# Performance work log

Hardware: AMD Instinct MI355X
Metric: run time of the kernel (lower is better)

Reference implementation:

```python
import jax, jax.numpy as jnp
import numpy as np

EPS = 1e-06
H = 25  # num heads


def _rmsnorm(x, w, eps=EPS):
    # normalize over last dim in float32, as in the torch module
    xf = x.astype(jnp.float32)
    var = jnp.mean(xf * xf, axis=-1, keepdims=True)
    return (w * (xf * jax.lax.rsqrt(var + eps))).astype(x.dtype)


def setup_inputs() -> dict:
    key = jax.random.key(0)
    ks = jax.random.split(key, 4)
    B, N, C = 8, 1025, 3200
    x = jax.random.normal(ks[0], (B, N, C), dtype=jnp.float32)
    qkv_w = jax.random.normal(ks[1], (C, 3 * C), dtype=jnp.float32) * (C ** -0.5)
    qkv_b = jnp.zeros((3 * C,), dtype=jnp.float32)
    q_norm_w = jnp.ones((C,), dtype=jnp.float32)
    k_norm_w = jnp.ones((C,), dtype=jnp.float32)
    proj_w = jax.random.normal(ks[2], (C, C), dtype=jnp.float32) * (C ** -0.5)
    proj_b = jnp.zeros((C,), dtype=jnp.float32)
    return {"x": x, "qkv_w": qkv_w, "qkv_b": qkv_b, "q_norm_w": q_norm_w,
            "k_norm_w": k_norm_w, "proj_w": proj_w, "proj_b": proj_b}


def reference(x, qkv_w, qkv_b, q_norm_w, k_norm_w, proj_w, proj_b):
    B, N, C = x.shape
    D = C // H
    scale = D ** -0.5
    qkv = x @ qkv_w + qkv_b                      # [B, N, 3C]
    q, k, v = jnp.split(qkv, 3, axis=-1)         # each [B, N, C]
    # QK RMSNorm is over the FULL embed_dim (heads flattened), per source.
    q = _rmsnorm(q, q_norm_w)
    k = _rmsnorm(k, k_norm_w)
    q = q.reshape(B, N, H, D)
    k = k.reshape(B, N, H, D)
    v = v.reshape(B, N, H, D)
    attn = jnp.einsum('bqhd,bkhd->bhqk', q * scale, k)   # [B, H, N, N]
    attn = jax.nn.softmax(attn, axis=-1)
    out = jnp.einsum('bhqk,bkhd->bqhd', attn, v).reshape(B, N, C)
    return out @ proj_w + proj_b
```

## Files before the change

### kernel.cpp

```cpp
#include <hip/hip_runtime.h>
#include <hip/hip_bf16.h>
#include <math.h>

#define B_ 8
#define N_ 1025
#define C_ 3200
#define H_ 25
#define D_ 128
#define M_ (B_ * N_)
#define C3_ (3 * C_)

typedef unsigned short u16;
typedef unsigned int u32;
typedef short bf16x8 __attribute__((ext_vector_type(8)));
typedef float f32x4 __attribute__((ext_vector_type(4)));

__device__ inline void load_lds16(const void* g, void* s) {
    __builtin_amdgcn_global_load_lds(
        (const __attribute__((address_space(1))) void*)g,
        (__attribute__((address_space(3))) void*)s, 16, 0, 0);
}

__device__ inline void split_pair(float x0, float x1, u32& hpk, u32& lpk) {
    __hip_bfloat162 h2 = __float22bfloat162_rn(float2{x0, x1});
    union { __hip_bfloat162 b; u32 u; } cv; cv.b = h2;
    u32 h = cv.u;
    float hf0 = __uint_as_float(h << 16);
    float hf1 = __uint_as_float(h & 0xFFFF0000u);
    __hip_bfloat162 l2 = __float22bfloat162_rn(float2{x0 - hf0, x1 - hf1});
    union { __hip_bfloat162 b; u32 u; } cl; cl.b = l2;
    hpk = h; lpk = cl.u;
}

__device__ inline void split1(float x, u16& h, u16& l) {
    union { __hip_bfloat16 b; u16 u; } ch, cl;
    ch.b = __float2bfloat16(x);
    float hf = __uint_as_float(((u32)ch.u) << 16);
    cl.b = __float2bfloat16(x - hf);
    h = ch.u; l = cl.u;
}

__global__ __launch_bounds__(256) void gemm_split(
    const float* __restrict__ A, const float* __restrict__ Bm,
    const float* __restrict__ bias, float* __restrict__ Cc,
    int M, int N)
{
    __shared__ u16  As_hi[128 * 32];
    __shared__ u16  As_lo[128 * 32];
    __shared__ float Bf[32 * 128];

    const int tid  = threadIdx.x;
    const int lane = tid & 63;
    const int w    = tid >> 6;
    const int wm   = w & 1, wn = w >> 1;
    const int rowBase = blockIdx.y * 128;
    const int colBase = blockIdx.x * 128;
    const int lr = lane & 15, lg = lane >> 4;

    const int ar = tid >> 3;
    const int ak = (tid & 7) * 4;

    f32x4 acc[4][4] = {};

    for (int k0 = 0; k0 < C_; k0 += 32) {
        #pragma unroll
        for (int p = 0; p < 4; ++p) {
            int c = p * 256 + tid;
            const float* g = Bm + (size_t)(k0 + (c >> 5)) * N
                                + colBase + (c & 31) * 4;
            load_lds16(g, &Bf[(p * 256 + w * 64) * 4]);
        }
        #pragma unroll
        for (int p = 0; p < 4; ++p) {
            int r  = p * 32 + ar;
            int gr = rowBase + r; if (gr >= M) gr = M - 1;
            float4 a4 = *(const float4*)(A + (size_t)gr * C_ + k0 + ak);
            u32 h0, h1, l0, l1;
            split_pair(a4.x, a4.y, h0, l0);
            split_pair(a4.z, a4.w, h1, l1);
            *(uint2*)&As_hi[r * 32 + ak] = make_uint2(h0, h1);
            *(uint2*)&As_lo[r * 32 + ak] = make_uint2(l0, l1);
        }
        __syncthreads();

        bf16x8 ah[4], al[4];
        #pragma unroll
        for (int i = 0; i < 4; ++i) {
            ah[i] = *(const bf16x8*)&As_hi[(wm * 64 + i * 16 + lr) * 32 + lg * 8];
            al[i] = *(const bf16x8*)&As_lo[(wm * 64 + i * 16 + lr) * 32 + lg * 8];
        }
        #pragma unroll
        for (int j = 0; j < 4; ++j) {
            const float* bp = &Bf[(lg * 8) * 128 + wn * 64 + j * 16 + lr];
            union { u32 u[4]; bf16x8 v; } BH, BL;
            split_pair(bp[0 * 128], bp[1 * 128], BH.u[0], BL.u[0]);
            split_pair(bp[2 * 128], bp[3 * 128], BH.u[1], BL.u[1]);
            split_pair(bp[4 * 128], bp[5 * 128], BH.u[2], BL.u[2]);
            split_pair(bp[6 * 128], bp[7 * 128], BH.u[3], BL.u[3]);
            #pragma unroll
            for (int i = 0; i < 4; ++i)
                acc[i][j] = __builtin_amdgcn_mfma_f32_16x16x32_bf16(
                    ah[i], BH.v, acc[i][j], 0, 0, 0);
            #pragma unroll
            for (int i = 0; i < 4; ++i)
                acc[i][j] = __builtin_amdgcn_mfma_f32_16x16x32_bf16(
                    al[i], BH.v, acc[i][j], 0, 0, 0);
            #pragma unroll
            for (int i = 0; i < 4; ++i)
                acc[i][j] = __builtin_amdgcn_mfma_f32_16x16x32_bf16(
                    ah[i], BL.v, acc[i][j], 0, 0, 0);
        }
        __syncthreads();
    }

    #pragma unroll
    for (int i = 0; i < 4; ++i) {
        #pragma unroll
        for (int j = 0; j < 4; ++j) {
            int gc = colBase + wn * 64 + j * 16 + lr;
            float bv = bias[gc];
            #pragma unroll
            for (int r = 0; r < 4; ++r) {
                int gr = rowBase + wm * 64 + i * 16 + lg * 4 + r;
                if (gr < M) Cc[(size_t)gr * N + gc] = acc[i][j][r] + bv;
            }
        }
    }
}

__global__ __launch_bounds__(256) void rmsnorm_kernel(
    float* __restrict__ qkv, const float* __restrict__ qw,
    const float* __restrict__ kw)
{
    const int row   = blockIdx.x >> 1;
    const int which = blockIdx.x & 1;
    float* p = qkv + (size_t)row * C3_ + which * C_;
    const float* w = which ? kw : qw;
    const int tid = threadIdx.x;

    float ss = 0.f;
    for (int i = tid; i < C_; i += 256) {
        float v = p[i];
        ss += v * v;
    }
    #pragma unroll
    for (int off = 32; off; off >>= 1) ss += __shfl_down(ss, off);

    __shared__ float wsum[4];
    __shared__ float stot;
    if ((tid & 63) == 0) wsum[tid >> 6] = ss;
    __syncthreads();
    if (tid == 0) stot = wsum[0] + wsum[1] + wsum[2] + wsum[3];
    __syncthreads();

    const float scale = rsqrtf(stot / (float)C_ + 1e-6f);
    for (int i = tid; i < C_; i += 256) p[i] = p[i] * scale * w[i];
}

__global__ __launch_bounds__(256, 2) void flash_mfma(
    const float* __restrict__ qkv, float* __restrict__ attn_out)
{
    __shared__ u16 Kh[4][32][32];
    __shared__ u16 Kl[4][32][32];
    __shared__ u16 Vth[128][40];
    __shared__ u16 Vtl[128][40];
    __shared__ u16 Ph[4][16][40];
    __shared__ u16 Pl[4][16][40];

    const int b   = blockIdx.z;
    const int h   = blockIdx.y;
    const int q0  = blockIdx.x * 64;
    const int tid = threadIdx.x;
    const int lane = tid & 63;
    const int w    = tid >> 6;
    const int lr = lane & 15, lg = lane >> 4;
    const float scale = 0.088388347648318447f;

    bf16x8 qh[4], ql[4];
    {
        int qr = q0 + w * 16 + lr;
        if (qr >= N_) qr = N_ - 1;
        const float* qp = qkv + (size_t)(b * N_ + qr) * C3_ + h * D_;
        #pragma unroll
        for (int c = 0; c < 4; ++c) {
            float4 x0 = *(const float4*)(qp + c * 32 + lg * 8);
            float4 x1 = *(const float4*)(qp + c * 32 + lg * 8 + 4);
            union { u32 u[4]; bf16x8 v; } Hq, Lq;
            split_pair(x0.x * scale, x0.y * scale, Hq.u[0], Lq.u[0]);
            split_pair(x0.z * scale, x0.w * scale, Hq.u[1], Lq.u[1]);
            split_pair(x1.x * scale, x1.y * scale, Hq.u[2], Lq.u[2]);
            split_pair(x1.z * scale, x1.w * scale, Hq.u[3], Lq.u[3]);
            qh[c] = Hq.v; ql[c] = Lq.v;
        }
    }

    const float* Kbase = qkv + (size_t)b * N_ * C3_ + C_ + h * D_;
    const float* Vbase = qkv + (size_t)b * N_ * C3_ + 2 * C_ + h * D_;

    const int skr = tid >> 3;
    const int skd = (tid & 7) * 16;
    const int svk = (tid & 15) * 2;
    const int svd = (tid >> 4) * 4;

    float4 kg[4], vg[2][2];

    auto stage_load = [&](int kt) {
        int kk = kt * 32 + skr;
        if (kk < N_) {
            const float* p = Kbase + (size_t)kk * C3_ + skd;
            kg[0] = *(const float4*)(p + 0);
            kg[1] = *(const float4*)(p + 4);
            kg[2] = *(const float4*)(p + 8);
            kg[3] = *(const float4*)(p + 12);
        } else {
            kg[0] = kg[1] = kg[2] = kg[3] = make_float4(0.f, 0.f, 0.f, 0.f);
        }
        #pragma unroll
        for (int r = 0; r < 2; ++r) {
            int vk = kt * 32 + svk + r;
            if (vk < N_) {
                const float* p = Vbase + (size_t)vk * C3_ + svd;
                vg[0][r] = *(const float4*)(p);
                vg[1][r] = *(const float4*)(p + 64);
            } else {
                vg[0][r] = make_float4(0.f, 0.f, 0.f, 0.f);
                vg[1][r] = make_float4(0.f, 0.f, 0.f, 0.f);
            }
        }
    };

    auto stage_store = [&]() {
        #pragma unroll
        for (int i = 0; i < 4; ++i) {
            int d = skd + i * 4;
            int c = d >> 5, dd = d & 31;
            u32 h0, l0, h1, l1;
            split_pair(kg[i].x, kg[i].y, h0, l0);
            split_pair(kg[i].z, kg[i].w, h1, l1);
            *(uint2*)&Kh[c][skr][dd] = make_uint2(h0, h1);
            *(uint2*)&Kl[c][skr][dd] = make_uint2(l0, l1);
        }
        #pragma unroll
        for (int half = 0; half < 2; ++half) {
            float a0[4] = { vg[half][0].x, vg[half][0].y, vg[half][0].z, vg[half][0].w };
            float a1[4] = { vg[half][1].x, vg[half][1].y, vg[half][1].z, vg[half][1].w };
            #pragma unroll
            for (int i = 0; i < 4; ++i) {
                int d = svd + half * 64 + i;
                u32 hp, lp;
                split_pair(a0[i], a1[i], hp, lp);
                *(u32*)&Vth[d][svk] = hp;
                *(u32*)&Vtl[d][svk] = lp;
            }
        }
    };

    f32x4 oacc[8] = {};
    float m[4]    = { -INFINITY, -INFINITY, -INFINITY, -INFINITY };
    float lsum[4] = { 0.f, 0.f, 0.f, 0.f };

    const int nkt = (N_ + 31) / 32;
    stage_load(0);
    for (int kt = 0; kt < nkt; ++kt) {
        __syncthreads();
        stage_store();
        __syncthreads();
        if (kt + 1 < nkt) stage_load(kt + 1);

        f32x4 s0 = {}, s1 = {};
        #pragma unroll
        for (int c = 0; c < 4; ++c) {
            bf16x8 kh0 = *(const bf16x8*)&Kh[c][lr][lg * 8];
            bf16x8 kl0 = *(const bf16x8*)&Kl[c][lr][lg * 8];
            bf16x8 kh1 = *(const bf16x8*)&Kh[c][16 + lr][lg * 8];
            bf16x8 kl1 = *(const bf16x8*)&Kl[c][16 + lr][lg * 8];
            s0 = __builtin_amdgcn_mfma_f32_16x16x32_bf16(qh[c], kh0, s0, 0, 0, 0);
            s0 = __builtin_amdgcn_mfma_f32_16x16x32_bf16(ql[c], kh0, s0, 0, 0, 0);
            s0 = __builtin_amdgcn_mfma_f32_16x16x32_bf16(qh[c], kl0, s0, 0, 0, 0);
            s1 = __builtin_amdgcn_mfma_f32_16x16x32_bf16(qh[c], kh1, s1, 0, 0, 0);
            s1 = __builtin_amdgcn_mfma_f32_16x16x32_bf16(ql[c], kh1, s1, 0, 0, 0);
            s1 = __builtin_amdgcn_mfma_f32_16x16x32_bf16(qh[c], kl1, s1, 0, 0, 0);
        }

        const int kb = kt * 32;
        const bool v0 = (kb + lr) < N_;
        const bool v1 = (kb + 16 + lr) < N_;
        #pragma unroll
        for (int r = 0; r < 4; ++r) {
            if (!v0) s0[r] = -INFINITY;
            if (!v1) s1[r] = -INFINITY;
        }

        #pragma unroll
        for (int r = 0; r < 4; ++r) {
            float mt = fmaxf(s0[r], s1[r]);
            mt = fmaxf(mt, __shfl_xor(mt, 1));
            mt = fmaxf(mt, __shfl_xor(mt, 2));
            mt = fmaxf(mt, __shfl_xor(mt, 4));
            mt = fmaxf(mt, __shfl_xor(mt, 8));
            float mn = fmaxf(m[r], mt);
            float al = __expf(m[r] - mn);
            m[r] = mn;
            float p0 = __expf(s0[r] - mn);
            float p1 = __expf(s1[r] - mn);
            float ls = p0 + p1;
            ls += __shfl_xor(ls, 1);
            ls += __shfl_xor(ls, 2);
            ls += __shfl_xor(ls, 4);
            ls += __shfl_xor(ls, 8);
            lsum[r] = lsum[r] * al + ls;
            #pragma unroll
            for (int dt = 0; dt < 8; ++dt) oacc[dt][r] *= al;

            u16 hh, ll;
            split1(p0, hh, ll);
            Ph[w][lg * 4 + r][lr] = hh;
            Pl[w][lg * 4 + r][lr] = ll;
            split1(p1, hh, ll);
            Ph[w][lg * 4 + r][16 + lr] = hh;
            Pl[w][lg * 4 + r][16 + lr] = ll;
        }

        bf16x8 pah = *(const bf16x8*)&Ph[w][lr][lg * 8];
        bf16x8 pal = *(const bf16x8*)&Pl[w][lr][lg * 8];
        #pragma unroll
        for (int dt = 0; dt < 8; ++dt) {
            bf16x8 vh = *(const bf16x8*)&Vth[dt * 16 + lr][lg * 8];
            bf16x8 vl = *(const bf16x8*)&Vtl[dt * 16 + lr][lg * 8];
            oacc[dt] = __builtin_amdgcn_mfma_f32_16x16x32_bf16(pah, vh, oacc[dt], 0, 0, 0);
            oacc[dt] = __builtin_amdgcn_mfma_f32_16x16x32_bf16(pal, vh, oacc[dt], 0, 0, 0);
            oacc[dt] = __builtin_amdgcn_mfma_f32_16x16x32_bf16(pah, vl, oacc[dt], 0, 0, 0);
        }
    }

    #pragma unroll
    for (int r = 0; r < 4; ++r) {
        int q = q0 + w * 16 + lg * 4 + r;
        if (q < N_) {
            float inv = 1.f / lsum[r];
            float* op = attn_out + (size_t)(b * N_ + q) * C_ + h * D_ + lr;
            #pragma unroll
            for (int dt = 0; dt < 8; ++dt) op[dt * 16] = oacc[dt][r] * inv;
        }
    }
}

extern "C" void kernel_launch(void* const* d_in, const int* in_sizes, int n_in,
                              void* d_out, int out_size, void* d_ws, size_t ws_size,
                              hipStream_t stream)
{
    const float* x        = (const float*)d_in[0];
    const float* qkv_w    = (const float*)d_in[1];
    const float* qkv_b    = (const float*)d_in[2];
    const float* q_norm_w = (const float*)d_in[3];
    const float* k_norm_w = (const float*)d_in[4];
    const float* proj_w   = (const float*)d_in[5];
    const float* proj_b   = (const float*)d_in[6];
    float* out = (float*)d_out;

    float* qkv      = (float*)d_ws;
    float* attn_out = qkv + (size_t)M_ * C3_;

    dim3 blk(256);

    gemm_split<<<dim3(C3_ / 128, (M_ + 127) / 128), blk, 0, stream>>>(
        x, qkv_w, qkv_b, qkv, M_, C3_);

    rmsnorm_kernel<<<dim3(M_ * 2), blk, 0, stream>>>(qkv, q_norm_w, k_norm_w);

    flash_mfma<<<dim3((N_ + 63) / 64, H_, B_), blk, 0, stream>>>(qkv, attn_out);

    gemm_split<<<dim3(C_ / 128, (M_ + 127) / 128), blk, 0, stream>>>(
        attn_out, proj_w, proj_b, out, M_, C_);
}
```

Measured before the change: 4.000 ms.

## Pre-split GEMM operands to bf16 hi/lo in workspace and use direct-to-LDS MFMA GEMM

New measurement: 3.999 ms. Within noise of the previous version (-0.0%).

```diff
diff --git a/kernel.cpp b/kernel.cpp
--- a/kernel.cpp
+++ b/kernel.cpp
@@ -40,6 +40,133 @@
     h = ch.u; l = cl.u;
 }
 
+__global__ __launch_bounds__(256) void convert_split(
+    const float4* __restrict__ in, uint2* __restrict__ hi,
+    uint2* __restrict__ lo, int n4)
+{
+    int i = blockIdx.x * 256 + threadIdx.x;
+    if (i < n4) {
+        float4 v = in[i];
+        u32 h0, l0, h1, l1;
+        split_pair(v.x, v.y, h0, l0);
+        split_pair(v.z, v.w, h1, l1);
+        hi[i] = make_uint2(h0, h1);
+        lo[i] = make_uint2(l0, l1);
+    }
+}
+
+__global__ __launch_bounds__(256) void convert_tsplit(
+    const float* __restrict__ in, u16* __restrict__ hi, u16* __restrict__ lo,
+    int K, int Nn)
+{
+    __shared__ float T[32][33];
+    const int tid = threadIdx.x;
+    const int nb = blockIdx.x * 32, kb = blockIdx.y * 32;
+    #pragma unroll
+    for (int p = 0; p < 4; ++p) {
+        int k = p * 8 + (tid >> 5), n = tid & 31;
+        T[k][n] = in[(size_t)(kb + k) * Nn + nb + n];
+    }
+    __syncthreads();
+    const int nn = tid >> 3, k0 = (tid & 7) * 4;
+    u32 h0, l0, h1, l1;
+    split_pair(T[k0][nn], T[k0 + 1][nn], h0, l0);
+    split_pair(T[k0 + 2][nn], T[k0 + 3][nn], h1, l1);
+    size_t o = (size_t)(nb + nn) * K + kb + k0;
+    *(uint2*)&hi[o] = make_uint2(h0, h1);
+    *(uint2*)&lo[o] = make_uint2(l0, l1);
+}
+
+__global__ __launch_bounds__(256) void gemm_bf16split(
+    const u16* __restrict__ Ah, const u16* __restrict__ Al,
+    const u16* __restrict__ Bh, const u16* __restrict__ Bl,
+    const float* __restrict__ bias, float* __restrict__ Cc,
+    int M, int N)
+{
+    __shared__ u16 As_h[4][128][8];
+    __shared__ u16 As_l[4][128][8];
+    __shared__ u16 Bs_h[4][128][8];
+    __shared__ u16 Bs_l[4][128][8];
+
+    const int tid  = threadIdx.x;
+    const int lane = tid & 63;
+    const int w    = tid >> 6;
+    const int wm   = w & 1, wn = w >> 1;
+    const int lr = lane & 15, lg = lane >> 4;
+
+    const int gX   = gridDim.x;
+    const int nwg  = gX * gridDim.y;
+    const int orig = blockIdx.y * gX + blockIdx.x;
+    const int q8 = nwg >> 3, r8 = nwg & 7;
+    const int xcd = orig & 7, oi = orig >> 3;
+    const int wg = (xcd < r8 ? xcd * (q8 + 1)
+                             : r8 * (q8 + 1) + (xcd - r8) * q8) + oi;
+    const int rowBase = (wg / gX) * 128;
+    const int colBase = (wg % gX) * 128;
+
+    f32x4 acc[4][4] = {};
+
+    for (int k0 = 0; k0 < C_; k0 += 32) {
+        #pragma unroll
+        for (int p = 0; p < 2; ++p) {
+            int c   = p * 256 + tid;
+            int row = c & 127, kc = c >> 7;
+            int ldsOff = (p * 256 + w * 64) * 8;
+            int ar = rowBase + row; if (ar >= M) ar = M - 1;
+            size_t aoff = (size_t)ar * C_ + k0 + kc * 8;
+            size_t boff = (size_t)(colBase + row) * C_ + k0 + kc * 8;
+            load_lds16(Ah + aoff, (u16*)As_h + ldsOff);
+            load_lds16(Al + aoff, (u16*)As_l + ldsOff);
+            load_lds16(Bh + boff, (u16*)Bs_h + ldsOff);
+            load_lds16(Bl + boff, (u16*)Bs_l + ldsOff);
+        }
+        __syncthreads();
+
+        bf16x8 ah[4], al[4], bh[4], bl[4];
+        #pragma unroll
+        for (int i = 0; i < 4; ++i) {
+            ah[i] = *(const bf16x8*)&As_h[lg][wm * 64 + i * 16 + lr][0];
+            al[i] = *(const bf16x8*)&As_l[lg][wm * 64 + i * 16 + lr][0];
+            bh[i] = *(const bf16x8*)&Bs_h[lg][wn * 64 + i * 16 + lr][0];
+            bl[i] = *(const bf16x8*)&Bs_l[lg][wn * 64 + i * 16 + lr][0];
+        }
+
+        #pragma unroll
+        for (int j = 0; j < 4; ++j)
+            #pragma unroll
+            for (int i = 0; i < 4; ++i)
+                acc[i][j] = __builtin_amdgcn_mfma_f32_16x16x32_bf16(
+                    ah[i], bh[j], acc[i][j], 0, 0, 0);
+        #pragma unroll
+        for (int j = 0; j < 4; ++j)
+            #pragma unroll
+            for (int i = 0; i < 4; ++i)
+                acc[i][j] = __builtin_amdgcn_mfma_f32_16x16x32_bf16(
+                    al[i], bh[j], acc[i][j], 0, 0, 0);
+        #pragma unroll
+        for (int j = 0; j < 4; ++j)
+            #pragma unroll
+            for (int i = 0; i < 4; ++i)
+                acc[i][j] = __builtin_amdgcn_mfma_f32_16x16x32_bf16(
+                    ah[i], bl[j], acc[i][j], 0, 0, 0);
+        __syncthreads();
+    }
+
+    #pragma unroll
+    for (int i = 0; i < 4; ++i) {
+        #pragma unroll
+        for (int j = 0; j < 4; ++j) {
+            int gc = colBase + wn * 64 + j * 16 + lr;
+            float bv = bias[gc];
+            #pragma unroll
+            for (int r = 0; r < 4; ++r) {
+                int gr = rowBase + wm * 64 + i * 16 + lg * 4 + r;
+                if (gr < M) Cc[(size_t)gr * N + gc] = acc[i][j][r] + bv;
+            }
+        }
+    }
+}
+
 __global__ __launch_bounds__(256) void gemm_split(
     const float* __restrict__ A, const float* __restrict__ Bm,
     const float* __restrict__ bias, float* __restrict__ Cc,
@@ -139,9 +266,9 @@
     const int tid = threadIdx.x;
 
     float ss = 0.f;
-    for (int i = tid; i < C_; i += 256) {
-        float v = p[i];
-        ss += v * v;
+    for (int i = tid; i < C_ / 4; i += 256) {
+        float4 v = ((const float4*)p)[i];
+        ss += v.x * v.x + v.y * v.y + v.z * v.z + v.w * v.w;
     }
     #pragma unroll
     for (int off = 32; off; off >>= 1) ss += __shfl_down(ss, off);
@@ -154,7 +281,13 @@
     __syncthreads();
 
     const float scale = rsqrtf(stot / (float)C_ + 1e-6f);
-    for (int i = tid; i < C_; i += 256) p[i] = p[i] * scale * w[i];
+    for (int i = tid; i < C_ / 4; i += 256) {
+        float4 v  = ((const float4*)p)[i];
+        float4 wv = ((const float4*)w)[i];
+        v.x *= scale * wv.x; v.y *= scale * wv.y;
+        v.z *= scale * wv.z; v.w *= scale * wv.w;
+        ((float4*)p)[i] = v;
+    }
 }
 
 __global__ __launch_bounds__(256, 2) void flash_mfma(
@@ -358,18 +491,50 @@
     const float* proj_b   = (const float*)d_in[6];
     float* out = (float*)d_out;
 
+    const size_t fQ = (size_t)M_ * C3_;
+    const size_t fA = (size_t)M_ * C_;
+    const size_t uW = (size_t)C3_ * C_;
+
     float* qkv      = (float*)d_ws;
-    float* attn_out = qkv + (size_t)M_ * C3_;
+    float* attn_out = qkv + fQ;
+
+    const size_t need = (fQ + fA) * 4 + fA * 2 * 2 + uW * 2 * 2;
 
     dim3 blk(256);
 
-    gemm_split<<<dim3(C3_ / 128, (M_ + 127) / 128), blk, 0, stream>>>(
-        x, qkv_w, qkv_b, qkv, M_, C3_);
-
-    rmsnorm_kernel<<<dim3(M_ * 2), blk, 0, stream>>>(qkv, q_norm_w, k_norm_w);
-
-    flash_mfma<<<dim3((N_ + 63) / 64, H_, B_), blk, 0, stream>>>(qkv, attn_out);
-
-    gemm_split<<<dim3(C_ / 128, (M_ + 127) / 128), blk, 0, stream>>>(
-        attn_out, proj_w, proj_b, out, M_, C_);
-}
+    if (ws_size >= need) {
+        u16* xh = (u16*)(attn_out + fA);
+        u16* xl = xh + fA;
+        u16* wh = xl + fA;
+        u16* wl = wh + uW;
+
+        const int n4 = (int)(fA / 4);
+
+        convert_split<<<dim3((n4 + 255) / 256), blk, 0, stream>>>(
+            (const float4*)x, (uint2*)xh, (uint2*)xl, n4);
+        convert_tsplit<<<dim3(C3_ / 32, C_ / 32), blk, 0, stream>>>(
+            qkv_w, wh, wl, C_, C3_);
+
+        gemm_bf16split<<<dim3(C3_ / 128, (M_ + 127) / 128), blk, 0, stream>>>(
+            xh, xl, wh, wl, qkv_b, qkv, M_, C3_);
+
+        rmsnorm_kernel<<<dim3(M_ * 2), blk, 0, stream>>>(qkv, q_norm_w, k_norm_w);
+
+        flash_mfma<<<dim3((N_ + 63) / 64, H_, B_), blk, 0, stream>>>(qkv, attn_out);
+
+        convert_split<<<dim3((n4 + 255) / 256), blk, 0, stream>>>(
+            (const float4*)attn_out, (uint2*)xh, (uint2*)xl, n4);
+        convert_tsplit<<<dim3(C_ / 32, C_ / 32), blk, 0, stream>>>(
+            proj_w, wh, wl, C_, C_);
+
+        gemm_bf16split<<<dim3(C_ / 128, (M_ + 127) / 128), blk, 0, stream>>>(
+            xh, xl, wh, wl, proj_b, out, M_, C_);
+    } else {
+        gemm_split<<<dim3(C3_ / 128, (M_ + 127) / 128), blk, 0, stream>>>(
+            x, qkv_w, qkv_b, qkv, M_, C3_);
+        rmsnorm_kernel<<<dim3(M_ * 2), blk, 0, stream>>>(qkv, q_norm_w, k_norm_w);
+        flash_mfma<<<dim3((N_ + 63) / 64, H_, B_), blk, 0, stream>>>(qkv, attn_out);
+        gemm_split<<<dim3(C_ / 128, (M_ + 127) / 128), blk, 0, stream>>>(
+            attn_out, proj_w, proj_b, out, M_, C_);
+    }
+}
```
